# Optimization experiments

Measured on AMD Instinct MI355X. Metric: run time of the kernel, lower is better.

Reference implementation:

```python
import jax, jax.numpy as jnp
import numpy as np

B, S, W = 64, 512, 16
E, TE, CE, CC = 300, 50, 50, 50
HID, TGT = 256, 16
VOCAB, TAGV, CHARV = 5002, 50, 100
IN = E + TE + CC  # 400


def setup_inputs() -> dict:
    key = jax.random.key(0)
    ks = jax.random.split(key, 24)
    sc = 0.1
    embed_table = (jax.random.normal(ks[0], (VOCAB, E)) * sc).at[0].set(0.0)
    tag_table = (jax.random.normal(ks[1], (TAGV, TE)) * sc).at[0].set(0.0)
    char_table = (jax.random.normal(ks[2], (CHARV, CE)) * sc).at[0].set(0.0)
    return {
        "X": jax.random.randint(ks[3], (B, S), 0, VOCAB),
        "labels_m": jax.random.uniform(ks[4], (B, S)),
        "tags": jax.random.randint(ks[5], (B, S), 0, TAGV),
        "chars": jax.random.randint(ks[6], (B, S, W), 0, CHARV),
        "embed_table": embed_table,
        "tag_table": tag_table,
        "char_table": char_table,
        "conv_w": jax.random.normal(ks[7], (CC, CE, 3)) * sc,
        "conv_b": jax.random.normal(ks[8], (CC,)) * sc,
        "w_ih_f": jax.random.normal(ks[9], (4 * HID, IN)) * sc,
        "w_hh_f": jax.random.normal(ks[10], (4 * HID, HID)) * sc,
        "b_ih_f": jax.random.normal(ks[11], (4 * HID,)) * sc,
        "b_hh_f": jax.random.normal(ks[12], (4 * HID,)) * sc,
        "w_ih_b": jax.random.normal(ks[13], (4 * HID, IN)) * sc,
        "w_hh_b": jax.random.normal(ks[14], (4 * HID, HID)) * sc,
        "b_ih_b": jax.random.normal(ks[15], (4 * HID,)) * sc,
        "b_hh_b": jax.random.normal(ks[16], (4 * HID,)) * sc,
        "fc_w": jax.random.normal(ks[17], (TGT, 2 * HID)) * sc,
        "fc_b": jax.random.normal(ks[18], (TGT,)) * sc,
        "A": jax.random.normal(ks[19], (TGT, TGT)),
        "wd": jax.random.normal(ks[20], (2 * HID,)),
    }


def _lstm_dir(xs, w_ih, w_hh, b_ih, b_hh, reverse):
    # xs: [S, B, IN] ; PyTorch gate order i,f,g,o
    h0 = jnp.zeros((xs.shape[1], w_hh.shape[1]), xs.dtype)

    def step(carry, x):
        h, c = carry
        g = x @ w_ih.T + h @ w_hh.T + (b_ih + b_hh)
        i, f, gg, o = jnp.split(g, 4, axis=-1)
        c = jax.nn.sigmoid(f) * c + jax.nn.sigmoid(i) * jnp.tanh(gg)
        h = jax.nn.sigmoid(o) * jnp.tanh(c)
        return (h, c), h

    _, hs = jax.lax.scan(step, (h0, h0), xs, reverse=reverse)
    return hs


def _features(X, labels_m, tags, chars, embed_table, tag_table, char_table,
              conv_w, conv_b, w_ih_f, w_hh_f, b_ih_f, b_hh_f,
              w_ih_b, w_hh_b, b_ih_b, b_hh_b, fc_w, fc_b, wd):
    embed = embed_table[X]          # [B,S,E]
    tag_embed = tag_table[tags]     # [B,S,TE]
    ce = char_table[chars]          # [B,S,W,CE]
    ce = ce.transpose(0, 3, 1, 2).reshape(B, CE, S * W)  # [B,CE,S*W]
    conv = jax.lax.conv_general_dilated(
        ce, conv_w, window_strides=(1,), padding=((1, 1),),
        dimension_numbers=("NCH", "OIH", "NCH")) + conv_b[None, :, None]
    char_conv = conv.reshape(B, CC, S, W).max(axis=3).transpose(0, 2, 1)  # [B,S,CC]
    feat = jnp.concatenate([embed, tag_embed, char_conv], axis=2)  # [B,S,IN]
    xs = feat.transpose(1, 0, 2)  # [S,B,IN]
    hf = _lstm_dir(xs, w_ih_f, w_hh_f, b_ih_f, b_hh_f, reverse=False)
    hb = _lstm_dir(xs, w_ih_b, w_hh_b, b_ih_b, b_hh_b, reverse=True)
    H = jnp.concatenate([hf, hb], axis=-1).transpose(1, 0, 2)  # [B,S,2H]
    H = H + labels_m[:, :, None] * wd[None, None, :]
    return H @ fc_w.T + fc_b  # [B,S,TGT]


def _viterbi(P, A):
    Xs = P.transpose(1, 0, 2)  # [S,B,T]
    b_idx = jnp.arange(P.shape[0])

    def vstep(delta, x):
        scores = delta[:, :, None] + A[None] + x[:, None, :]  # [B,prev,cur]
        return scores.max(axis=1), (scores.max(axis=1), scores.argmax(axis=1))

    deltaL, (drest, psis) = jax.lax.scan(vstep, Xs[0], Xs[1:])
    deltas = jnp.concatenate([Xs[0][None], drest], axis=0)  # [S,B,T]
    psi_end = deltaL.argmax(axis=1)                          # [B]
    score0 = deltaL[b_idx, psi_end]

    def back(carry, inp):
        tag, sc = carry
        psi_t, delta_t = inp
        prev = psi_t[b_idx, tag]
        return (prev, sc + delta_t[b_idx, prev]), prev

    (_, score), prevs = jax.lax.scan(back, (psi_end, score0),
                                     (psis, deltas[:-1]), reverse=True)
    path = jnp.concatenate([prevs, psi_end[None]], axis=0).T  # [B,S]
    return path, score


def reference(X, labels_m, tags, chars, embed_table, tag_table, char_table,
              conv_w, conv_b, w_ih_f, w_hh_f, b_ih_f, b_hh_f,
              w_ih_b, w_hh_b, b_ih_b, b_hh_b, fc_w, fc_b, A, wd):
    P = _features(X, labels_m, tags, chars, embed_table, tag_table, char_table,
                  conv_w, conv_b, w_ih_f, w_hh_f, b_ih_f, b_hh_f,
                  w_ih_b, w_hh_b, b_ih_b, b_hh_b, fc_w, fc_b, wd)
    return _viterbi(P, A)
```

## Files before the change

kernel.cpp:

```cpp
#include <hip/hip_runtime.h>


#define DEV __device__ __forceinline__
typedef unsigned short u16;
typedef unsigned int   u32;
typedef unsigned char  u8;
typedef signed char    s8;
using short8  = __attribute__((ext_vector_type(8))) short;
using f32x4   = __attribute__((ext_vector_type(4))) float;
using int4v   = __attribute__((ext_vector_type(4))) int;

DEV float bf2f(u16 u){ union{u32 i; float f;} v; v.i = ((u32)u)<<16; return v.f; }
DEV u16 f2bf(float f){ u32 x = __float_as_uint(f); return (u16)((x + 0x7fffu + ((x>>16)&1u)) >> 16); }
DEV float sigf(float x){ return __builtin_amdgcn_rcpf(1.f + __expf(-x)); }
DEV float tanh_f(float x){ return 1.f - 2.f*__builtin_amdgcn_rcpf(__expf(2.f*x) + 1.f); }

typedef __attribute__((address_space(1))) const u32 GU;
typedef __attribute__((address_space(3))) u32 LU;
DEV void gld_lds16(const void* g, void* l){
  __builtin_amdgcn_global_load_lds((GU*)g, (LU*)l, 16, 0, 0);
}
DEV void bar_l(){
  __builtin_amdgcn_sched_barrier(0);
  asm volatile("s_waitcnt lgkmcnt(0)" ::: "memory");
  __builtin_amdgcn_s_barrier();
  __builtin_amdgcn_sched_barrier(0);
}

static const size_t OFF_GI   = 0;
static const size_t OFF_P    = 0;
static const size_t OFF_DL   = OFF_P  + (size_t)32768*16*4;
static const size_t OFF_PSI  = OFF_DL + (size_t)32768*16*4;
static const size_t OFF_B    = (size_t)134217728;
static const size_t OFF_WIH  = OFF_B    + (size_t)33554432;
static const size_t OFF_WQ   = OFF_WIH  + (size_t)1703936;
static const size_t OFF_SC   = OFF_WQ   + (size_t)524288;
static const size_t OFF_BIAS = OFF_SC   + 8192;
static const size_t OFF_WFC  = OFF_BIAS + 8192;
static const size_t REQUIRED = OFF_WFC  + 256;

__global__ void k0_pack(const float* __restrict__ wihf, const float* __restrict__ wihb,
                        u16* __restrict__ wih)
{
  int n = blockIdx.x, tid = threadIdx.x;
  const float* src = (n < 1024) ? (wihf + (size_t)n*400) : (wihb + (size_t)(n-1024)*400);
  u32* dst = (u32*)(wih + (size_t)n*416);
  if (tid < 208){
    int j = tid*2;
    u32 v = 0u;
    if (j < 400){
      float2 f = *(const float2*)(src + j);
      v = (u32)f2bf(f.x) | ((u32)f2bf(f.y) << 16);
    }
    dst[tid] = v;
  }
}

__global__ __launch_bounds__(256) void k0q(
    const float* __restrict__ whhf, const float* __restrict__ whhb,
    s8* __restrict__ wq, float* __restrict__ sc2)
{
  const int row = blockIdx.x*4 + (threadIdx.x >> 6);
  const int lane = threadIdx.x & 63;
  const float* src = (row < 1024) ? (whhf + (size_t)row*256)
                                  : (whhb + (size_t)(row-1024)*256);
  f32x4 v = *(const f32x4*)(src + lane*4);
  float m = fmaxf(fmaxf(fabsf(v[0]), fabsf(v[1])), fmaxf(fabsf(v[2]), fabsf(v[3])));
  #pragma unroll
  for (int d = 1; d < 64; d <<= 1) m = fmaxf(m, __shfl_xor(m, d, 64));
  float inv = 127.f / (m + 1e-30f);
  u32 pack = 0;
  #pragma unroll
  for (int e = 0; e < 4; e++){
    int q = (int)rintf(v[e]*inv);
    q = q > 127 ? 127 : (q < -127 ? -127 : q);
    pack |= ((u32)(u8)(s8)q) << (8*e);
  }
  const int dir = row >> 10, n = row & 1023;
  const int g = n >> 8, j = n & 255, w2 = j >> 4, lr2 = j & 15;
  const int kk = lane >> 4, lq2 = (lane >> 2) & 3, e4 = lane & 3;
  u32* wq32 = (u32*)wq;
  wq32[dir*65536 + (((g*16 + w2)*4 + kk)*64 + lq2*16 + lr2)*4 + e4] = pack;
  if (lane == 0) sc2[row] = m * (1.f/16129.f);
}

__global__ void k0_misc(const float* bihf, const float* bhhf, const float* bihb, const float* bhhb,
                        const float* fcw, const float* wdp, float* bias, float* wfc)
{
  __shared__ float red[256];
  int tid = threadIdx.x;
  for (int n = tid; n < 2048; n += 256){
    bias[n] = (n < 1024) ? (bihf[n] + bhhf[n]) : (bihb[n-1024] + bhhb[n-1024]);
  }
  const int cur = tid & 15, part = tid >> 4;
  float s = 0.f;
  for (int k = part*32; k < part*32 + 32; k++) s += fcw[cur*512 + k] * wdp[k];
  red[tid] = s;
  __syncthreads();
  if (tid < 16){
    float t = 0.f;
    #pragma unroll
    for (int p = 0; p < 16; p++) t += red[p*16 + tid];
    wfc[tid] = t;
  }
}

__global__ __launch_bounds__(256) void k1_feat(
    const int* __restrict__ X, const int* __restrict__ tg, const int* __restrict__ ch,
    const float* __restrict__ etab, const float* __restrict__ ttab, const float* __restrict__ ctab,
    const float* __restrict__ cw, const float* __restrict__ cb, u16* __restrict__ feat)
{
  const int sb = blockIdx.x, b = blockIdx.y, tid = threadIdx.x;
  __shared__ float ce_s[66*60];
  __shared__ float w_s[150*52];
  for (int i = tid; i < 600; i += 256){
    int wl = i/150, j = i - wl*150;
    int s = sb*4 + wl;
    int idx = X[b*512 + s];
    float2 f = *(const float2*)(etab + (size_t)idx*300 + j*2);
    *(u32*)(feat + (size_t)(s*64 + b)*416 + j*2) = (u32)f2bf(f.x) | ((u32)f2bf(f.y) << 16);
  }
  for (int i = tid; i < 100; i += 256){
    int wl = i/25, j = i - wl*25;
    int s = sb*4 + wl;
    int idx = tg[b*512 + s];
    float2 f = *(const float2*)(ttab + (size_t)idx*50 + j*2);
    *(u32*)(feat + (size_t)(s*64 + b)*416 + 300 + j*2) = (u32)f2bf(f.x) | ((u32)f2bf(f.y) << 16);
  }
  if (tid < 32){
    int wl = tid>>3, j = tid&7;
    int s = sb*4 + wl;
    *(u32*)(feat + (size_t)(s*64 + b)*416 + 400 + j*2) = 0u;
  }
  for (int i = tid; i < 3300; i += 256){
    int qq = i/50, ce = i - qq*50;
    int p = sb*64 - 1 + qq;
    float v = 0.f;
    if (p >= 0 && p < 8192){
      int ci = ch[b*8192 + p];
      v = ctab[ci*50 + ce];
    }
    ce_s[qq*60 + ce] = v;
  }
  for (int i = tid; i < 7500; i += 256){
    int cc = i/150, r2 = i - cc*150;
    int ce = r2/3, dc = r2 - ce*3;
    w_s[(cc*3 + dc)*52 + ce] = cw[i];
  }
  __syncthreads();
  const int li = tid & 15, jg = tid >> 4;
  float acc[4][3];
  #pragma unroll
  for (int k=0;k<4;k++){ acc[k][0]=0.f; acc[k][1]=0.f; acc[k][2]=0.f; }
  #pragma unroll
  for (int dc = 0; dc < 3; dc++){
    for (int ceb = 0; ceb < 48; ceb += 4){
      f32x4 w0 = *(const f32x4*)&w_s[((3*jg+0)*3 + dc)*52 + ceb];
      f32x4 w1 = *(const f32x4*)&w_s[((3*jg+1)*3 + dc)*52 + ceb];
      f32x4 w2 = *(const f32x4*)&w_s[((3*jg+2)*3 + dc)*52 + ceb];
      #pragma unroll
      for (int k = 0; k < 4; k++){
        f32x4 cv = *(const f32x4*)&ce_s[(16*k + li + dc)*60 + ceb];
        #pragma unroll
        for (int e = 0; e < 4; e++){
          acc[k][0] += cv[e]*w0[e];
          acc[k][1] += cv[e]*w1[e];
          acc[k][2] += cv[e]*w2[e];
        }
      }
    }
    float w0a = w_s[((3*jg+0)*3+dc)*52 + 48], w0b = w_s[((3*jg+0)*3+dc)*52 + 49];
    float w1a = w_s[((3*jg+1)*3+dc)*52 + 48], w1b = w_s[((3*jg+1)*3+dc)*52 + 49];
    float w2a = w_s[((3*jg+2)*3+dc)*52 + 48], w2b = w_s[((3*jg+2)*3+dc)*52 + 49];
    #pragma unroll
    for (int k = 0; k < 4; k++){
      float ca = ce_s[(16*k + li + dc)*60 + 48];
      float cb2 = ce_s[(16*k + li + dc)*60 + 49];
      acc[k][0] += ca*w0a + cb2*w0b;
      acc[k][1] += ca*w1a + cb2*w1b;
      acc[k][2] += ca*w2a + cb2*w2b;
    }
  }
  #pragma unroll
  for (int m = 1; m < 16; m <<= 1)
    #pragma unroll
    for (int k=0;k<4;k++)
      #pragma unroll
      for (int c=0;c<3;c++)
        acc[k][c] = fmaxf(acc[k][c], __shfl_xor(acc[k][c], m, 64));
  if (li == 0){
    #pragma unroll
    for (int k=0;k<4;k++)
      #pragma unroll
      for (int c=0;c<3;c++){
        int cc = 3*jg + c;
        int s = sb*4 + k;
        feat[(size_t)(s*64 + b)*416 + 350 + cc] = f2bf(acc[k][c] + cb[cc]);
      }
  }
  if (tid < 128){
    int pl = tid & 63, cc = 48 + (tid >> 6);
    float a2 = 0.f;
    #pragma unroll
    for (int dc = 0; dc < 3; dc++){
      for (int ceb = 0; ceb < 48; ceb += 4){
        f32x4 wv = *(const f32x4*)&w_s[(cc*3 + dc)*52 + ceb];
        f32x4 cv = *(const f32x4*)&ce_s[(pl + dc)*60 + ceb];
        a2 += cv[0]*wv[0] + cv[1]*wv[1] + cv[2]*wv[2] + cv[3]*wv[3];
      }
      a2 += ce_s[(pl+dc)*60 + 48]*w_s[(cc*3+dc)*52 + 48]
          + ce_s[(pl+dc)*60 + 49]*w_s[(cc*3+dc)*52 + 49];
    }
    #pragma unroll
    for (int m = 1; m < 16; m <<= 1) a2 = fmaxf(a2, __shfl_xor(a2, m, 64));
    if ((tid & 15) == 0){
      int s = sb*4 + ((tid & 63) >> 4);
      feat[(size_t)(s*64 + b)*416 + 350 + cc] = f2bf(a2 + cb[cc]);
    }
  }
}

__global__ __launch_bounds__(256) void k2_gemm(
    const u16* __restrict__ featp, const u16* __restrict__ wihp,
    const float* __restrict__ bias, u16* __restrict__ gi)
{
  const int m0 = blockIdx.y*128, n0 = blockIdx.x*128;
  const int tid = threadIdx.x, wv = tid>>6, lane = tid&63;
  const int lr = lane & 15, lq = lane >> 4;
  const int wm = (wv>>1)*64, wn = (wv&1)*64;
  __shared__ u16 As[4096], Bs[4096];
  f32x4 acc[4][4];
  #pragma unroll
  for (int a=0;a<4;a++)
    #pragma unroll
    for (int c=0;c<4;c++) acc[a][c] = (f32x4){0.f,0.f,0.f,0.f};
  for (int k0 = 0; k0 < 416; k0 += 32){
    __syncthreads();
    #pragma unroll
    for (int i = 0; i < 2; i++){
      int c = i*4 + wv;
      gld_lds16(featp + (size_t)(m0 + c*16 + (lane>>2))*416 + k0 + (lane&3)*8, &As[c*512]);
      gld_lds16(wihp  + (size_t)(n0 + c*16 + (lane>>2))*416 + k0 + (lane&3)*8, &Bs[c*512]);
    }
    __syncthreads();
    short8 af[4], bfr[4];
    #pragma unroll
    for (int mt=0; mt<4; mt++) af[mt]  = *(const short8*)(As + (wm + mt*16 + lr)*32 + lq*8);
    #pragma unroll
    for (int nt=0; nt<4; nt++) bfr[nt] = *(const short8*)(Bs + (wn + nt*16 + lr)*32 + lq*8);
    #pragma unroll
    for (int mt=0; mt<4; mt++)
      #pragma unroll
      for (int nt=0; nt<4; nt++)
        acc[mt][nt] = __builtin_amdgcn_mfma_f32_16x16x32_bf16(af[mt], bfr[nt], acc[mt][nt], 0,0,0);
  }
  #pragma unroll
  for (int nt=0; nt<4; nt++){
    float bv = bias[n0 + wn + nt*16 + lr];
    #pragma unroll
    for (int mt=0; mt<4; mt++)
      #pragma unroll
      for (int r=0; r<4; r++)
        gi[(size_t)(m0 + wm + mt*16 + lq*4 + r)*2048 + n0 + wn + nt*16 + lr]
            = f2bf(acc[mt][nt][r] + bv);
  }
}

__global__ __launch_bounds__(512, 2) void k3_lstm(
    const s8* __restrict__ wq, const float* __restrict__ sc2,
    const u16* __restrict__ gi, u16* __restrict__ hcat)
{
  const int dir = blockIdx.x >> 5;
  const int bb  = (blockIdx.x & 31) * 2;
  const int tid = threadIdx.x;
  const int w = tid >> 6, lane = tid & 63;
  const int lr = lane & 15, lq = lane >> 4;
  const int cb = tid >> 8, cj = tid & 255;

  __shared__ s8 Hs[2][4096];
  __shared__ float xbuf[2048];

  const s8* wqd = wq + dir*262144;
  int4v bq[2][4][4];
  #pragma unroll
  for (int sl = 0; sl < 2; sl++)
    #pragma unroll
    for (int g = 0; g < 4; g++)
      #pragma unroll
      for (int kk = 0; kk < 4; kk++)
        bq[sl][g][kk] = *(const int4v*)(wqd + (((((g*16 + 2*w + sl)*4 + kk)*64) + lane) << 4));

  float scl[4];
  #pragma unroll
  for (int g = 0; g < 4; g++) scl[g] = sc2[dir*1024 + g*256 + cj];

  *(uint2*)&Hs[0][tid*8] = (uint2){0u,0u};
  *(uint2*)&Hs[1][tid*8] = (uint2){0u,0u};

  float cst = 0.f;
  const ptrdiff_t dstep = dir ? -(ptrdiff_t)131072 : (ptrdiff_t)131072;
  const u16* g0 = gi + (size_t)((dir ? 511 : 0)*64 + bb + cb)*2048 + dir*1024 + cj;
  u32 gcur[4], gn1[4], gn2[4];
  #pragma unroll
  for (int g = 0; g < 4; g++) gcur[g] = g0[g*256];
  const u16* g1 = g0 + dstep;
  #pragma unroll
  for (int g = 0; g < 4; g++) gn1[g] = g1[g*256];
  const u16* gpref = g1;
  __syncthreads();

  #pragma unroll 1
  for (int t = 0; t < 512; t++){
    const int s = dir ? (511 - t) : t;
    if (t + 2 < 512) gpref += dstep;
    #pragma unroll
    for (int g = 0; g < 4; g++) gn2[g] = gpref[g*256];
    const s8* hb = Hs[t & 1];
    int4v aq[4];
    #pragma unroll
    for (int kk = 0; kk < 4; kk++)
      aq[kk] = *(const int4v*)(hb + lr*256 + ((kk*64 + lq*16) ^ (lr << 4)));
    int4v acc[2][4];
    #pragma unroll
    for (int sl = 0; sl < 2; sl++)
      #pragma unroll
      for (int g = 0; g < 4; g++) acc[sl][g] = (int4v){0,0,0,0};
    #pragma unroll
    for (int kk = 0; kk < 4; kk++)
      #pragma unroll
      for (int sl = 0; sl < 2; sl++)
        #pragma unroll
        for (int g = 0; g < 4; g++)
          acc[sl][g] = __builtin_amdgcn_mfma_i32_16x16x64_i8(aq[kk], bq[sl][g][kk], acc[sl][g], 0,0,0);
    if (lq == 0){
      #pragma unroll
      for (int sl = 0; sl < 2; sl++){
        const int j = (2*w + sl)*16 + lr;
        #pragma unroll
        for (int r = 0; r < 2; r++){
          f32x4 v = (f32x4){(float)acc[sl][0][r], (float)acc[sl][1][r],
                            (float)acc[sl][2][r], (float)acc[sl][3][r]};
          *(f32x4*)&xbuf[(r*256 + j)*4] = v;
        }
      }
    }
    bar_l();
    f32x4 p = *(const f32x4*)&xbuf[tid*4];
    float g4[4];
    #pragma unroll
    for (int g = 0; g < 4; g++) g4[g] = bf2f((u16)gcur[g]) + p[g]*scl[g];
    float iv = sigf(g4[0]), fv = sigf(g4[1]);
    float gg = tanh_f(g4[2]), ov = sigf(g4[3]);
    float c = fv*cst + iv*gg;
    cst = c;
    float h = ov * tanh_f(c);
    hcat[(size_t)(s*64 + bb + cb)*512 + dir*256 + cj] = f2bf(h);
    int q = (int)rintf(h * 127.f);
    Hs[(t + 1) & 1][cb*256 + (cj ^ (cb << 4))] = (s8)q;
    #pragma unroll
    for (int g = 0; g < 4; g++){ gcur[g] = gn1[g]; gn1[g] = gn2[g]; }
    bar_l();
  }
}

__global__ __launch_bounds__(256) void k4_fc(
    const u16* __restrict__ hcat, const float* __restrict__ fcw, const float* __restrict__ fcb,
    const float* __restrict__ lmp, const float* __restrict__ wfc, float* __restrict__ Pout)
{
  const int wv = threadIdx.x >> 6, lane = threadIdx.x & 63;
  const int lr = lane & 15, lq = lane >> 4;
  const int mt = blockIdx.x*4 + wv;
  short8 bfr[16];
  #pragma unroll
  for (int kk = 0; kk < 16; kk++){
    const float* wr = fcw + (size_t)lr*512 + kk*32 + lq*8;
    f32x4 w0 = *(const f32x4*)wr;
    f32x4 w1 = *(const f32x4*)(wr + 4);
    short8 sv;
    #pragma unroll
    for (int e = 0; e < 4; e++){ sv[e] = (short)f2bf(w0[e]); sv[4+e] = (short)f2bf(w1[e]); }
    bfr[kk] = sv;
  }
  f32x4 acc = (f32x4){0.f,0.f,0.f,0.f};
  #pragma unroll
  for (int kk = 0; kk < 16; kk++){
    short8 af = *(const short8*)(hcat + (size_t)(mt*16 + lr)*512 + kk*32 + lq*8);
    acc = __builtin_amdgcn_mfma_f32_16x16x32_bf16(af, bfr[kk], acc, 0,0,0);
  }
  const int cur = lr;
  float fb = fcb[cur];
  float wf = wfc[cur];
  #pragma unroll
  for (int r = 0; r < 4; r++){
    int m = mt*16 + lq*4 + r;
    int b = m & 63, s = m >> 6;
    float lmv = lmp[b*512 + s];
    Pout[(size_t)m*16 + cur] = acc[r] + fb + lmv*wf;
  }
}

__global__ __launch_bounds__(64) void k5_vit(
    const float* __restrict__ Pg, const float* __restrict__ Am,
    float* __restrict__ dout, float* __restrict__ dl, u8* __restrict__ psi)
{
  const int b = blockIdx.x, lane = threadIdx.x;
  const int cur = lane >> 2, q = lane & 3;
  float Ar[4];
  #pragma unroll
  for (int r = 0; r < 4; r++) Ar[r] = Am[(4*q + r)*16 + cur];
  float val = Pg[(size_t)b*16 + cur];
  if (q == 0) dl[(size_t)b*16 + cur] = val;

#define FSTEP(X, S) { \
    float best = -3.0e38f; int bi = 0; \
    _Pragma("unroll") \
    for (int r = 0; r < 4; r++){ \
      float dp = __shfl(val, (4*q + r)*4, 64); \
      float sc = (dp + Ar[r]) + (X); \
      if (sc > best){ best = sc; bi = 4*q + r; } \
    } \
    { float ov = __shfl_xor(best, 1, 64); int oi = __shfl_xor(bi, 1, 64); \
      if (ov > best || (ov == best && oi < bi)){ best = ov; bi = oi; } } \
    { float ov = __shfl_xor(best, 2, 64); int oi = __shfl_xor(bi, 2, 64); \
      if (ov > best || (ov == best && oi < bi)){ best = ov; bi = oi; } } \
    val = best; \
    if (q == 0){ \
      dl[(size_t)((S)*64 + b)*16 + cur] = best; \
      psi[(size_t)((S)*64 + b)*16 + cur] = (u8)bi; \
    } }

  float x0 = Pg[(size_t)(1*64 + b)*16 + cur];
  float x1 = Pg[(size_t)(2*64 + b)*16 + cur];
  float x2 = Pg[(size_t)(3*64 + b)*16 + cur];
  float x3 = Pg[(size_t)(4*64 + b)*16 + cur];
  for (int s = 1; s < 512; s += 4){
    FSTEP(x0, s);
    if (s + 4 < 512) x0 = Pg[(size_t)((s+4)*64 + b)*16 + cur];
    if (s + 1 < 512) FSTEP(x1, s+1);
    if (s + 5 < 512) x1 = Pg[(size_t)((s+5)*64 + b)*16 + cur];
    if (s + 2 < 512) FSTEP(x2, s+2);
    if (s + 6 < 512) x2 = Pg[(size_t)((s+6)*64 + b)*16 + cur];
    if (s + 3 < 512) FSTEP(x3, s+3);
    if (s + 7 < 512) x3 = Pg[(size_t)((s+7)*64 + b)*16 + cur];
  }
#undef FSTEP

  float bv = val; int bix = cur;
  #pragma unroll
  for (int m = 1; m < 64; m <<= 1){
    float ov = __shfl_xor(bv, m, 64);
    int   oi = __shfl_xor(bix, m, 64);
    if (ov > bv || (ov == bv && oi < bix)){ bv = ov; bix = oi; }
  }
  int tag = bix;
  float score = bv;
  if (lane == 0) dout[b*512 + 511] = (float)tag;

#define BSTEP(PV, DV, T) { \
    int prev = __shfl((PV), tag, 64); \
    score += __shfl((DV), prev, 64); \
    if (lane == 0) dout[b*512 + (T)] = (float)prev; \
    tag = prev; }

  int   p0 = 0, p1 = 0, p2 = 0, p3 = 0;
  float d0 = 0.f, d1 = 0.f, d2 = 0.f, d3 = 0.f;
  if (lane < 16){
    p0 = psi[(size_t)(511*64 + b)*16 + lane]; d0 = dl[(size_t)(510*64 + b)*16 + lane];
    p1 = psi[(size_t)(510*64 + b)*16 + lane]; d1 = dl[(size_t)(509*64 + b)*16 + lane];
    p2 = psi[(size_t)(509*64 + b)*16 + lane]; d2 = dl[(size_t)(508*64 + b)*16 + lane];
    p3 = psi[(size_t)(508*64 + b)*16 + lane]; d3 = dl[(size_t)(507*64 + b)*16 + lane];
  }
  for (int t = 510; t >= 0; t -= 4){
    BSTEP(p0, d0, t);
    if (t - 4 >= 0 && lane < 16){
      p0 = psi[(size_t)((t-3)*64 + b)*16 + lane]; d0 = dl[(size_t)((t-4)*64 + b)*16 + lane];
    }
    if (t - 1 >= 0) BSTEP(p1, d1, t-1);
    if (t - 5 >= 0 && lane < 16){
      p1 = psi[(size_t)((t-4)*64 + b)*16 + lane]; d1 = dl[(size_t)((t-5)*64 + b)*16 + lane];
    }
    if (t - 2 >= 0) BSTEP(p2, d2, t-2);
    if (t - 6 >= 0 && lane < 16){
      p2 = psi[(size_t)((t-5)*64 + b)*16 + lane]; d2 = dl[(size_t)((t-6)*64 + b)*16 + lane];
    }
    if (t - 3 >= 0) BSTEP(p3, d3, t-3);
    if (t - 7 >= 0 && lane < 16){
      p3 = psi[(size_t)((t-6)*64 + b)*16 + lane]; d3 = dl[(size_t)((t-7)*64 + b)*16 + lane];
    }
  }
#undef BSTEP
  if (lane == 0) dout[32768 + b] = score;
}

extern "C" void kernel_launch(void* const* d_in, const int* in_sizes, int n_in,
                              void* d_out, int out_size, void* d_ws, size_t ws_size,
                              hipStream_t stream)
{
  (void)in_sizes; (void)n_in; (void)out_size;
  if (ws_size < REQUIRED) return;

  const int*   X    = (const int*)d_in[0];
  const float* lm   = (const float*)d_in[1];
  const int*   tg   = (const int*)d_in[2];
  const int*   ch   = (const int*)d_in[3];
  const float* etab = (const float*)d_in[4];
  const float* ttab = (const float*)d_in[5];
  const float* ctab = (const float*)d_in[6];
  const float* cw   = (const float*)d_in[7];
  const float* cb   = (const float*)d_in[8];
  const float* wihf = (const float*)d_in[9];
  const float* whhf = (const float*)d_in[10];
  const float* bihf = (const float*)d_in[11];
  const float* bhhf = (const float*)d_in[12];
  const float* wihb = (const float*)d_in[13];
  const float* whhb = (const float*)d_in[14];
  const float* bihb = (const float*)d_in[15];
  const float* bhhb = (const float*)d_in[16];
  const float* fcw  = (const float*)d_in[17];
  const float* fcb  = (const float*)d_in[18];
  const float* Am   = (const float*)d_in[19];
  const float* wdp  = (const float*)d_in[20];

  char* ws = (char*)d_ws;
  u16*   gi   = (u16*)(ws + OFF_GI);
  u16*   feat = (u16*)(ws + OFF_B);
  u16*   hcat = (u16*)(ws + OFF_B);
  u16*   wih  = (u16*)(ws + OFF_WIH);
  s8*    wq   = (s8*)(ws + OFF_WQ);
  float* sc2  = (float*)(ws + OFF_SC);
  float* Pg   = (float*)(ws + OFF_P);
  float* dlt  = (float*)(ws + OFF_DL);
  u8*    psi  = (u8*)(ws + OFF_PSI);
  float* bias = (float*)(ws + OFF_BIAS);
  float* wfc  = (float*)(ws + OFF_WFC);
  float* dout = (float*)d_out;

  k0_pack<<<2048, 256, 0, stream>>>(wihf, wihb, wih);
  k0q<<<512, 256, 0, stream>>>(whhf, whhb, wq, sc2);
  k0_misc<<<1, 256, 0, stream>>>(bihf, bhhf, bihb, bhhb, fcw, wdp, bias, wfc);
  k1_feat<<<dim3(128, 64), 256, 0, stream>>>(X, tg, ch, etab, ttab, ctab, cw, cb, feat);
  k2_gemm<<<dim3(16, 256), 256, 0, stream>>>(feat, wih, bias, gi);
  k3_lstm<<<64, 512, 0, stream>>>(wq, sc2, gi, hcat);
  k4_fc<<<512, 256, 0, stream>>>(hcat, fcw, fcb, lm, wfc, Pg);
  k5_vit<<<64, 64, 0, stream>>>(Pg, Am, dout, dlt, psi);
}
```

Before: 1.173 ms.

## Fuse LSTM gate activation into MFMA lanes and drop mid-step barrier

The LSTM recurrence kernel no longer stages integer gate accumulators through an LDS buffer with an extra barrier. The lanes that hold MFMA results (lq==0) now apply the scale, input gates, activations and cell update directly, then write h. The input-projection GEMM writes its output gate-interleaved per hidden unit, so each active lane fetches all four gates with one vector load. This removes one barrier and an LDS round trip per timestep, but leaves only a quarter of the lanes doing the serial nonlinear math, four cells each.

```diff
diff --git a/kernel.cpp b/kernel.cpp
--- a/kernel.cpp
+++ b/kernel.cpp
@@ -7,6 +7,7 @@
 typedef unsigned char  u8;
 typedef signed char    s8;
 using short8  = __attribute__((ext_vector_type(8))) short;
+using ushort4v= __attribute__((ext_vector_type(4))) unsigned short;
 using f32x4   = __attribute__((ext_vector_type(4))) float;
 using int4v   = __attribute__((ext_vector_type(4))) int;
 
@@ -256,13 +257,18 @@
   }
   #pragma unroll
   for (int nt=0; nt<4; nt++){
-    float bv = bias[n0 + wn + nt*16 + lr];
+    const int n = n0 + wn + nt*16 + lr;
+    const float bv = bias[n];
+    const int dirn = n >> 10, g = (n >> 8) & 3, j = n & 255;
     #pragma unroll
     for (int mt=0; mt<4; mt++)
       #pragma unroll
-      for (int r=0; r<4; r++)
-        gi[(size_t)(m0 + wm + mt*16 + lq*4 + r)*2048 + n0 + wn + nt*16 + lr]
+      for (int r=0; r<4; r++){
+        const int m = m0 + wm + mt*16 + lq*4 + r;
+        const int s = m >> 6, b = m & 63;
+        gi[((size_t)((dirn*512 + s)*64 + b) << 10) + (j << 2) + g]
             = f2bf(acc[mt][nt][r] + bv);
+      }
   }
 }
 
@@ -275,10 +281,8 @@
   const int tid = threadIdx.x;
   const int w = tid >> 6, lane = tid & 63;
   const int lr = lane & 15, lq = lane >> 4;
-  const int cb = tid >> 8, cj = tid & 255;
 
   __shared__ s8 Hs[2][4096];
-  __shared__ float xbuf[2048];
 
   const s8* wqd = wq + dir*262144;
   int4v bq[2][4][4];
@@ -290,31 +294,46 @@
       for (int kk = 0; kk < 4; kk++)
         bq[sl][g][kk] = *(const int4v*)(wqd + (((((g*16 + 2*w + sl)*4 + kk)*64) + lane) << 4));
 
-  float scl[4];
-  #pragma unroll
-  for (int g = 0; g < 4; g++) scl[g] = sc2[dir*1024 + g*256 + cj];
+  const bool act = (lq == 0);
+  const int jb = 2*w*16 + lr;
+
+  float scl2[2][4];
+  #pragma unroll
+  for (int sl = 0; sl < 2; sl++)
+    #pragma unroll
+    for (int g = 0; g < 4; g++)
+      scl2[sl][g] = sc2[dir*1024 + g*256 + jb + sl*16];
 
   *(uint2*)&Hs[0][tid*8] = (uint2){0u,0u};
   *(uint2*)&Hs[1][tid*8] = (uint2){0u,0u};
 
-  float cst = 0.f;
-  const ptrdiff_t dstep = dir ? -(ptrdiff_t)131072 : (ptrdiff_t)131072;
-  const u16* g0 = gi + (size_t)((dir ? 511 : 0)*64 + bb + cb)*2048 + dir*1024 + cj;
-  u32 gcur[4], gn1[4], gn2[4];
-  #pragma unroll
-  for (int g = 0; g < 4; g++) gcur[g] = g0[g*256];
-  const u16* g1 = g0 + dstep;
-  #pragma unroll
-  for (int g = 0; g < 4; g++) gn1[g] = g1[g*256];
-  const u16* gpref = g1;
+  float cst[2][2] = {{0.f,0.f},{0.f,0.f}};
+  const ptrdiff_t dstep = dir ? -(ptrdiff_t)65536 : (ptrdiff_t)65536;
+  const u16* gp = gi + ((size_t)((dir*512 + (dir ? 511 : 0))*64 + bb) << 10);
+  ushort4v gc[2][2], g1r[2][2], g2r[2][2];
+  if (act){
+    #pragma unroll
+    for (int sl = 0; sl < 2; sl++)
+      #pragma unroll
+      for (int r = 0; r < 2; r++){
+        gc[sl][r]  = *(const ushort4v*)(gp + r*1024 + (jb + sl*16)*4);
+        g1r[sl][r] = *(const ushort4v*)(gp + dstep + r*1024 + (jb + sl*16)*4);
+      }
+  }
+  const u16* gpref = gp + dstep;
   __syncthreads();
 
   #pragma unroll 1
   for (int t = 0; t < 512; t++){
     const int s = dir ? (511 - t) : t;
     if (t + 2 < 512) gpref += dstep;
-    #pragma unroll
-    for (int g = 0; g < 4; g++) gn2[g] = gpref[g*256];
+    if (act){
+      #pragma unroll
+      for (int sl = 0; sl < 2; sl++)
+        #pragma unroll
+        for (int r = 0; r < 2; r++)
+          g2r[sl][r] = *(const ushort4v*)(gpref + r*1024 + (jb + sl*16)*4);
+    }
     const s8* hb = Hs[t & 1];
     int4v aq[4];
     #pragma unroll
@@ -332,33 +351,31 @@
         #pragma unroll
         for (int g = 0; g < 4; g++)
           acc[sl][g] = __builtin_amdgcn_mfma_i32_16x16x64_i8(aq[kk], bq[sl][g][kk], acc[sl][g], 0,0,0);
-    if (lq == 0){
+    if (act){
+      s8* hw = Hs[(t + 1) & 1];
       #pragma unroll
       for (int sl = 0; sl < 2; sl++){
-        const int j = (2*w + sl)*16 + lr;
+        const int j = jb + sl*16;
         #pragma unroll
         for (int r = 0; r < 2; r++){
-          f32x4 v = (f32x4){(float)acc[sl][0][r], (float)acc[sl][1][r],
-                            (float)acc[sl][2][r], (float)acc[sl][3][r]};
-          *(f32x4*)&xbuf[(r*256 + j)*4] = v;
+          float g4[4];
+          #pragma unroll
+          for (int g = 0; g < 4; g++)
+            g4[g] = bf2f((u16)gc[sl][r][g]) + (float)acc[sl][g][r] * scl2[sl][g];
+          float iv = sigf(g4[0]), fv = sigf(g4[1]);
+          float gg = tanh_f(g4[2]), ov = sigf(g4[3]);
+          float c = fv*cst[sl][r] + iv*gg;
+          cst[sl][r] = c;
+          float h = ov * tanh_f(c);
+          hcat[(size_t)(s*64 + bb + r)*512 + dir*256 + j] = f2bf(h);
+          hw[r*256 + (j ^ (r << 4))] = (s8)(int)rintf(h * 127.f);
         }
       }
-    }
-    bar_l();
-    f32x4 p = *(const f32x4*)&xbuf[tid*4];
-    float g4[4];
-    #pragma unroll
-    for (int g = 0; g < 4; g++) g4[g] = bf2f((u16)gcur[g]) + p[g]*scl[g];
-    float iv = sigf(g4[0]), fv = sigf(g4[1]);
-    float gg = tanh_f(g4[2]), ov = sigf(g4[3]);
-    float c = fv*cst + iv*gg;
-    cst = c;
-    float h = ov * tanh_f(c);
-    hcat[(size_t)(s*64 + bb + cb)*512 + dir*256 + cj] = f2bf(h);
-    int q = (int)rintf(h * 127.f);
-    Hs[(t + 1) & 1][cb*256 + (cj ^ (cb << 4))] = (s8)q;
-    #pragma unroll
-    for (int g = 0; g < 4; g++){ gcur[g] = gn1[g]; gn1[g] = gn2[g]; }
+      #pragma unroll
+      for (int sl = 0; sl < 2; sl++)
+        #pragma unroll
+        for (int r = 0; r < 2; r++){ gc[sl][r] = g1r[sl][r]; g1r[sl][r] = g2r[sl][r]; }
+    }
     bar_l();
   }
 }
```

Result: slower. 1.392 ms (+18.7%).

## Make LSTM gate combine wave-local and interleave gate layout in precomputed input projections

Applied to the files above, without the earlier changes.

Each wave in the recurrent LSTM kernel now applies the gate nonlinearities for exactly the hidden units and batch rows its own MFMAs produced. The cross-wave exchange through shared memory therefore needs only an LDS wait instead of a full workgroup barrier, leaving one barrier per time step instead of two. The input-projection GEMM now stores its output per direction and time step with the four gates of each hidden unit adjacent. This lets each thread fetch its four gate pre-activations with a single 8-byte load instead of four scattered 2-byte loads. The price is a more scattered store pattern in the GEMM epilogue.

```diff
diff --git a/kernel.cpp b/kernel.cpp
--- a/kernel.cpp
+++ b/kernel.cpp
@@ -7,6 +7,7 @@
 typedef unsigned char  u8;
 typedef signed char    s8;
 using short8  = __attribute__((ext_vector_type(8))) short;
+using ushort4v= __attribute__((ext_vector_type(4))) unsigned short;
 using f32x4   = __attribute__((ext_vector_type(4))) float;
 using int4v   = __attribute__((ext_vector_type(4))) int;
 
@@ -24,6 +25,11 @@
   __builtin_amdgcn_sched_barrier(0);
   asm volatile("s_waitcnt lgkmcnt(0)" ::: "memory");
   __builtin_amdgcn_s_barrier();
+  __builtin_amdgcn_sched_barrier(0);
+}
+DEV void lgkm0(){
+  __builtin_amdgcn_sched_barrier(0);
+  asm volatile("s_waitcnt lgkmcnt(0)" ::: "memory");
   __builtin_amdgcn_sched_barrier(0);
 }
 
@@ -256,13 +262,18 @@
   }
   #pragma unroll
   for (int nt=0; nt<4; nt++){
-    float bv = bias[n0 + wn + nt*16 + lr];
+    const int n = n0 + wn + nt*16 + lr;
+    const float bv = bias[n];
+    const int dirn = n >> 10, g = (n >> 8) & 3, j = n & 255;
     #pragma unroll
     for (int mt=0; mt<4; mt++)
       #pragma unroll
-      for (int r=0; r<4; r++)
-        gi[(size_t)(m0 + wm + mt*16 + lq*4 + r)*2048 + n0 + wn + nt*16 + lr]
+      for (int r=0; r<4; r++){
+        const int m = m0 + wm + mt*16 + lq*4 + r;
+        const int s = m >> 6, b = m & 63;
+        gi[((size_t)((dirn*512 + s)*64 + b) << 10) + (j << 2) + g]
             = f2bf(acc[mt][nt][r] + bv);
+      }
   }
 }
 
@@ -275,10 +286,9 @@
   const int tid = threadIdx.x;
   const int w = tid >> 6, lane = tid & 63;
   const int lr = lane & 15, lq = lane >> 4;
-  const int cb = tid >> 8, cj = tid & 255;
 
   __shared__ s8 Hs[2][4096];
-  __shared__ float xbuf[2048];
+  __shared__ float xbuf[8][2][32][4];
 
   const s8* wqd = wq + dir*262144;
   int4v bq[2][4][4];
@@ -290,31 +300,31 @@
       for (int kk = 0; kk < 4; kk++)
         bq[sl][g][kk] = *(const int4v*)(wqd + (((((g*16 + 2*w + sl)*4 + kk)*64) + lane) << 4));
 
+  const int r_own = lane >> 5;
+  const int jloc  = lane & 31;
+  const int j_own = 2*w*16 + jloc;
+
   float scl[4];
   #pragma unroll
-  for (int g = 0; g < 4; g++) scl[g] = sc2[dir*1024 + g*256 + cj];
+  for (int g = 0; g < 4; g++) scl[g] = sc2[dir*1024 + g*256 + j_own];
 
   *(uint2*)&Hs[0][tid*8] = (uint2){0u,0u};
   *(uint2*)&Hs[1][tid*8] = (uint2){0u,0u};
 
   float cst = 0.f;
-  const ptrdiff_t dstep = dir ? -(ptrdiff_t)131072 : (ptrdiff_t)131072;
-  const u16* g0 = gi + (size_t)((dir ? 511 : 0)*64 + bb + cb)*2048 + dir*1024 + cj;
-  u32 gcur[4], gn1[4], gn2[4];
-  #pragma unroll
-  for (int g = 0; g < 4; g++) gcur[g] = g0[g*256];
-  const u16* g1 = g0 + dstep;
-  #pragma unroll
-  for (int g = 0; g < 4; g++) gn1[g] = g1[g*256];
-  const u16* gpref = g1;
+  const ptrdiff_t dstep = dir ? -(ptrdiff_t)65536 : (ptrdiff_t)65536;
+  const u16* gp = gi + ((size_t)((dir*512 + (dir ? 511 : 0))*64 + bb + r_own) << 10) + j_own*4;
+  ushort4v gc, g1, g2;
+  gc = *(const ushort4v*)gp;
+  g1 = *(const ushort4v*)(gp + dstep);
+  const u16* gpref = gp + dstep;
   __syncthreads();
 
   #pragma unroll 1
   for (int t = 0; t < 512; t++){
     const int s = dir ? (511 - t) : t;
     if (t + 2 < 512) gpref += dstep;
-    #pragma unroll
-    for (int g = 0; g < 4; g++) gn2[g] = gpref[g*256];
+    g2 = *(const ushort4v*)gpref;
     const s8* hb = Hs[t & 1];
     int4v aq[4];
     #pragma unroll
@@ -334,31 +344,27 @@
           acc[sl][g] = __builtin_amdgcn_mfma_i32_16x16x64_i8(aq[kk], bq[sl][g][kk], acc[sl][g], 0,0,0);
     if (lq == 0){
       #pragma unroll
-      for (int sl = 0; sl < 2; sl++){
-        const int j = (2*w + sl)*16 + lr;
+      for (int sl = 0; sl < 2; sl++)
         #pragma unroll
         for (int r = 0; r < 2; r++){
           f32x4 v = (f32x4){(float)acc[sl][0][r], (float)acc[sl][1][r],
                             (float)acc[sl][2][r], (float)acc[sl][3][r]};
-          *(f32x4*)&xbuf[(r*256 + j)*4] = v;
+          *(f32x4*)&xbuf[w][r][sl*16 + lr][0] = v;
         }
-      }
-    }
-    bar_l();
-    f32x4 p = *(const f32x4*)&xbuf[tid*4];
+    }
+    lgkm0();
+    f32x4 p = *(const f32x4*)&xbuf[w][r_own][jloc][0];
     float g4[4];
     #pragma unroll
-    for (int g = 0; g < 4; g++) g4[g] = bf2f((u16)gcur[g]) + p[g]*scl[g];
+    for (int g = 0; g < 4; g++) g4[g] = bf2f((u16)gc[g]) + p[g]*scl[g];
     float iv = sigf(g4[0]), fv = sigf(g4[1]);
     float gg = tanh_f(g4[2]), ov = sigf(g4[3]);
     float c = fv*cst + iv*gg;
     cst = c;
     float h = ov * tanh_f(c);
-    hcat[(size_t)(s*64 + bb + cb)*512 + dir*256 + cj] = f2bf(h);
-    int q = (int)rintf(h * 127.f);
-    Hs[(t + 1) & 1][cb*256 + (cj ^ (cb << 4))] = (s8)q;
-    #pragma unroll
-    for (int g = 0; g < 4; g++){ gcur[g] = gn1[g]; gn1[g] = gn2[g]; }
+    hcat[(size_t)(s*64 + bb + r_own)*512 + dir*256 + j_own] = f2bf(h);
+    Hs[(t + 1) & 1][r_own*256 + (j_own ^ (r_own << 4))] = (s8)(int)rintf(h * 127.f);
+    gc = g1; g1 = g2;
     bar_l();
   }
 }
```

Result: slower. 1.260 ms (+7.4%).
